# Performance work log

Hardware: AMD Instinct MI355X
Metric: run time of the kernel (lower is better)

Reference implementation:

```python
import jax, jax.numpy as jnp
import numpy as np

EPS = 1e-5

@jax.custom_vjp
def binarize(x):
    # sign with sign(0)->+1, as in typical BNN implementations
    return jnp.where(x >= 0, 1.0, -1.0).astype(x.dtype)

def _bin_fwd(x):
    return binarize(x), x

def _bin_bwd(x, g):
    # hardtanh straight-through estimator
    return (g * (jnp.abs(x) <= 1.0).astype(g.dtype),)

binarize.defvjp(_bin_fwd, _bin_bwd)

def bconv3x3(x, w, stride=1):
    bx = binarize(x)
    bw = binarize(w)
    return jax.lax.conv_general_dilated(
        bx, bw, window_strides=(stride, stride), padding=[(1, 1), (1, 1)],
        dimension_numbers=("NCHW", "OIHW", "NCHW"))

def bn(x, gamma, beta, mean, var):
    inv = gamma / jnp.sqrt(var + EPS)
    return x * inv[None, :, None, None] + (beta - mean * inv)[None, :, None, None]

def channel_shuffle(x, groups=2):
    b, c, h, w = x.shape
    x = x.reshape(b, groups, c // groups, h, w)
    x = jnp.transpose(x, (0, 2, 1, 3, 4))
    return x.reshape(b, c, h, w)

def hardtanh(x):
    return jnp.clip(x, -1.0, 1.0)

def setup_inputs() -> dict:
    key = jax.random.key(0)
    ks = jax.random.split(key, 13)
    P = 128
    inp = {
        "x": jax.random.normal(ks[0], (32, 2 * P, 56, 56), jnp.float32),
        "w1": jax.random.normal(ks[1], (P, P, 3, 3), jnp.float32) * 0.05,
        "w2": jax.random.normal(ks[2], (P, P, 3, 3), jnp.float32) * 0.05,
        "bn1_gamma": jax.random.uniform(ks[3], (P,), jnp.float32, 0.5, 1.5),
        "bn1_beta": jax.random.normal(ks[4], (P,), jnp.float32) * 0.1,
        "bn1_mean": jax.random.normal(ks[5], (P,), jnp.float32),
        "bn1_var": jax.random.uniform(ks[6], (P,), jnp.float32, 0.5, 1.5),
        "bn2_gamma": jax.random.uniform(ks[7], (P,), jnp.float32, 0.5, 1.5),
        "bn2_beta": jax.random.normal(ks[8], (P,), jnp.float32) * 0.1,
        "bn2_mean": jax.random.normal(ks[9], (P,), jnp.float32),
        "bn2_var": jax.random.uniform(ks[10], (P,), jnp.float32, 0.5, 1.5),
        "move0_bias": jax.random.normal(ks[11], (P,), jnp.float32) * 0.01,
        "move1_bias": jax.random.normal(ks[12], (P,), jnp.float32) * 0.01,
    }
    return inp

def reference(x, w1, w2, bn1_gamma, bn1_beta, bn1_mean, bn1_var,
              bn2_gamma, bn2_beta, bn2_mean, bn2_var, move0_bias, move1_bias):
    P = w1.shape[0]
    # split into active / idle halves
    x_act, x_idle = x[:, :P], x[:, P:]
    residual = x_act
    out = bn(bconv3x3(x_act, w1, stride=1), bn1_gamma, bn1_beta, bn1_mean, bn1_var)
    out = hardtanh(out + residual)
    x_idle = x_idle + move0_bias[None, :, None, None]
    out = channel_shuffle(jnp.concatenate([out, x_idle], axis=1))
    x_act2, x_idle2 = out[:, :P], out[:, P:]
    residual = x_act2
    out = bn(bconv3x3(x_act2, w2, stride=1), bn2_gamma, bn2_beta, bn2_mean, bn2_var)
    out = hardtanh(out + residual)
    x_idle2 = x_idle2 + move1_bias[None, :, None, None]
    out = channel_shuffle(jnp.concatenate([out, x_idle2], axis=1))
    return out
```

## Files before the change

kernel.cpp:

```cpp
#include <hip/hip_runtime.h>
#include <stdint.h>


#define HH 56
#define WW 56
#define HW 3136
#define NBATCH 32
#define NPX (NBATCH * HW)

#define WS_W1B   0u
#define WS_W2B   18432u
#define WS_BN    36864u
#define WS_BITS2 40960u
#define WS_BITS1 1646592u
#define WS_RES1  3252224u

#define PC(a,b) (__popc((a).x ^ (b).x) + __popc((a).y ^ (b).y) + \
                 __popc((a).z ^ (b).z) + __popc((a).w ^ (b).w))

__global__ __launch_bounds__(256) void binpack_kernel(
    const float* __restrict__ x, const float* __restrict__ move0,
    const float* __restrict__ move1,
    const float* __restrict__ w1, const float* __restrict__ w2,
    const float* __restrict__ g1, const float* __restrict__ b1,
    const float* __restrict__ m1, const float* __restrict__ v1,
    const float* __restrict__ g2, const float* __restrict__ b2,
    const float* __restrict__ m2, const float* __restrict__ v2,
    uint4* __restrict__ bits1, uint4* __restrict__ bits2,
    uint4* __restrict__ w1b, uint4* __restrict__ w2b, float* __restrict__ bnc,
    float* __restrict__ out)
{
    if (blockIdx.x >= 1960) {
        int t = (blockIdx.x - 1960) * 256 + threadIdx.x;
        if (t < 2304) {
            const float* w = (t < 1152) ? w1 : w2;
            uint4* dst = (t < 1152) ? w1b : w2b;
            int tt = (t < 1152) ? t : t - 1152;
            int o = tt / 9, tap = tt % 9;
            const float* wp = w + (size_t)o * 1152 + tap;
            uint32_t b[4];
            #pragma unroll
            for (int wd = 0; wd < 4; ++wd) {
                uint32_t acc = 0;
                #pragma unroll
                for (int bi = 0; bi < 32; ++bi) {
                    float wv = wp[(size_t)(wd * 32 + bi) * 9];
                    acc |= (wv >= 0.0f ? 1u : 0u) << bi;
                }
                b[wd] = acc;
            }
            dst[o * 9 + tap] = make_uint4(b[0], b[1], b[2], b[3]);
        } else if (t < 2432) {
            int c = t - 2304;
            float i1 = __fdiv_rn(g1[c], __fsqrt_rn(__fadd_rn(v1[c], 1e-5f)));
            bnc[c]       = i1;
            bnc[128 + c] = __fsub_rn(b1[c], __fmul_rn(m1[c], i1));
            float i2 = __fdiv_rn(g2[c], __fsqrt_rn(__fadd_rn(v2[c], 1e-5f)));
            bnc[256 + c] = i2;
            bnc[384 + c] = __fsub_rn(b2[c], __fmul_rn(m2[c], i2));
        }
        return;
    }

    const int g = blockIdx.x / 392;
    const int px = (blockIdx.x % 392) * 256 + threadIdx.x;
    const int n = px / HW, poff = px % HW;
    const float* xn = x + (size_t)n * 256 * HW + poff;

    if (g < 2) {
        const int cb = g * 64;
        uint32_t w0 = 0, w1v = 0;
        #pragma unroll
        for (int c = 0; c < 32; ++c)
            w0 |= (xn[(size_t)(cb + c) * HW] >= 0.0f ? 1u : 0u) << c;
        #pragma unroll
        for (int c = 0; c < 32; ++c)
            w1v |= (xn[(size_t)(cb + 32 + c) * HW] >= 0.0f ? 1u : 0u) << c;
        ((uint2*)&bits1[px])[g] = make_uint2(w0, w1v);
    } else if (g == 2) {
        uint32_t w0 = 0, w1v = 0, w2v = 0, w3 = 0;
        #pragma unroll
        for (int k = 0; k < 64; ++k) {
            float s = __fadd_rn(xn[(size_t)(128 + k) * HW], move0[k]);
            uint32_t m = (s >= 0.0f ? 1u : 0u) << (2 * (k & 15) + 1);
            if ((k >> 4) == 0) w0 |= m; else if ((k >> 4) == 1) w1v |= m;
            else if ((k >> 4) == 2) w2v |= m; else w3 |= m;
        }
        bits2[px] = make_uint4(w0, w1v, w2v, w3);
    } else {
        const int mb = (g - 3) * 32;
        for (int mm = 0; mm < 32; ++mm) {
            int m = mb + mm;
            float v = __fadd_rn(__fadd_rn(xn[(size_t)(192 + m) * HW],
                                          move0[64 + m]), move1[2 * m + 1]);
            __builtin_nontemporal_store(v,
                &out[(size_t)(n * 256 + 4 * m + 3) * HW + poff]);
        }
    }
}


__device__ __forceinline__ int clampi(int v, int lo, int hi) {
    return v < lo ? lo : (v > hi ? hi : v);
}

__global__ __launch_bounds__(256) void conv1_kernel(
    const float* __restrict__ x, const uint4* __restrict__ w1b,
    const float* __restrict__ bnc, const float* __restrict__ move1,
    const uint4* __restrict__ bits1, uint4* __restrict__ bits2,
    uint2* __restrict__ res1, float* __restrict__ out)
{
    const int b = blockIdx.x;
    const int js = b & 15;
    const int px = (b >> 4) * 256 + threadIdx.x;
    const int n = px / HW, poff = px % HW;

    const float* xn = x + (size_t)n * 256 * HW;
    const size_t pxi = (size_t)px;
    const uint4* __restrict__ wjs = w1b + js * 72;

    float rres[8];
    #pragma unroll
    for (int jj = 0; jj < 8; ++jj)
        rres[jj] = xn[(size_t)(js * 8 + jj) * HW + poff];
    uint32_t old16 = 0;
    if (js < 8) old16 = ((const uint16_t*)(bits2 + pxi))[js];

    const int row = poff / WW, col = poff % WW;
    const int rok0 = (row >= 1), rok2 = (row <= HH - 2);
    const int cok0 = (col >= 1), cok2 = (col <= WW - 2);
    const uint32_t rs0 = rok0 ? ~0u : 0u, rs2 = rok2 ? ~0u : 0u;
    const uint32_t csL = cok0 ? ~0u : 0u, csR = cok2 ? ~0u : 0u;
    const int nvbase = ((1 + rok0 + rok2) * (1 + cok0 + cok2)) << 7;

    const uint4* bsrc = bits1 + (size_t)n * HW;
    const uint4 i00 = bsrc[clampi(poff - 57, 0, HW - 1)];
    const uint4 i01 = bsrc[clampi(poff - 56, 0, HW - 1)];
    const uint4 i02 = bsrc[clampi(poff - 55, 0, HW - 1)];
    const uint4 i10 = bsrc[clampi(poff - 1, 0, HW - 1)];
    const uint4 i11 = bsrc[poff];
    const uint4 i12 = bsrc[clampi(poff + 1, 0, HW - 1)];
    const uint4 i20 = bsrc[clampi(poff + 55, 0, HW - 1)];
    const uint4 i21 = bsrc[clampi(poff + 56, 0, HW - 1)];
    const uint4 i22 = bsrc[clampi(poff + 57, 0, HW - 1)];

    uint32_t bw = old16;
    uint32_t q0 = 0, q1 = 0;

    #pragma unroll
    for (int jj = 0; jj < 8; ++jj) {
        const int j = js * 8 + jj;
        int acc = 0;
        acc += PC(wjs[jj * 9 + 0], i00) & (int)(rs0 & csL);
        acc += PC(wjs[jj * 9 + 1], i01) & (int)rs0;
        acc += PC(wjs[jj * 9 + 2], i02) & (int)(rs0 & csR);
        acc += PC(wjs[jj * 9 + 3], i10) & (int)csL;
        acc += PC(wjs[jj * 9 + 4], i11);
        acc += PC(wjs[jj * 9 + 5], i12) & (int)csR;
        acc += PC(wjs[jj * 9 + 6], i20) & (int)(rs2 & csL);
        acc += PC(wjs[jj * 9 + 7], i21) & (int)rs2;
        acc += PC(wjs[jj * 9 + 8], i22) & (int)(rs2 & csR);
        float convf = (float)(nvbase - (acc << 1));
        float bno = __fadd_rn(__fmul_rn(convf, bnc[j]), bnc[128 + j]);
        float v2 = __fadd_rn(bno, rres[jj]);
        float vc = fminf(fmaxf(v2, -1.0f), 1.0f);
        if (js < 8) {
            bw |= (v2 >= 0.0f ? 1u : 0u) << (2 * jj);
            uint32_t q = (uint32_t)(uint8_t)(int8_t)__float2int_rn(
                __fmul_rn(vc, 127.0f));
            uint32_t sh = 8 * (jj & 3);
            if (jj < 4) q0 |= q << sh; else q1 |= q << sh;
        } else {
            int m = j - 64;
            __builtin_nontemporal_store(__fadd_rn(vc, move1[2 * m]),
                &out[(size_t)(n * 256 + 4 * m + 1) * HW + poff]);
        }
    }
    if (js < 8) {
        res1[(size_t)js * NPX + pxi] = make_uint2(q0, q1);
        ((uint16_t*)(bits2 + pxi))[js] = (uint16_t)bw;
    }
}

__global__ __launch_bounds__(256) void conv2_kernel(
    const float* __restrict__ x, const uint4* __restrict__ w2b,
    const float* __restrict__ bnc, const float* __restrict__ move0,
    const uint4* __restrict__ bits2, const uint2* __restrict__ res1,
    float* __restrict__ out)
{
    const int b = blockIdx.x;
    const int js = b & 15;
    const int px = (b >> 4) * 256 + threadIdx.x;
    const int n = px / HW, poff = px % HW;

    const float* xn = x + (size_t)n * 256 * HW;
    const size_t pxi = (size_t)px;
    const uint4* __restrict__ wjs = w2b + js * 72;

    const uint32_t rq = ((const uint32_t*)(res1 + (size_t)(js >> 1) * NPX + pxi))[js & 1];
    float ro[4];
    #pragma unroll
    for (int k = 0; k < 4; ++k)
        ro[k] = xn[(size_t)(128 + js * 4 + k) * HW + poff];

    const int row = poff / WW, col = poff % WW;
    const int rok0 = (row >= 1), rok2 = (row <= HH - 2);
    const int cok0 = (col >= 1), cok2 = (col <= WW - 2);
    const uint32_t rs0 = rok0 ? ~0u : 0u, rs2 = rok2 ? ~0u : 0u;
    const uint32_t csL = cok0 ? ~0u : 0u, csR = cok2 ? ~0u : 0u;
    const int nvbase = ((1 + rok0 + rok2) * (1 + cok0 + cok2)) << 7;

    const uint4* bsrc = bits2 + (size_t)n * HW;
    const uint4 i00 = bsrc[clampi(poff - 57, 0, HW - 1)];
    const uint4 i01 = bsrc[clampi(poff - 56, 0, HW - 1)];
    const uint4 i02 = bsrc[clampi(poff - 55, 0, HW - 1)];
    const uint4 i10 = bsrc[clampi(poff - 1, 0, HW - 1)];
    const uint4 i11 = bsrc[poff];
    const uint4 i12 = bsrc[clampi(poff + 1, 0, HW - 1)];
    const uint4 i20 = bsrc[clampi(poff + 55, 0, HW - 1)];
    const uint4 i21 = bsrc[clampi(poff + 56, 0, HW - 1)];
    const uint4 i22 = bsrc[clampi(poff + 57, 0, HW - 1)];

    #pragma unroll
    for (int jj = 0; jj < 8; ++jj) {
        const int j = js * 8 + jj;
        int acc = 0;
        acc += PC(wjs[jj * 9 + 0], i00) & (int)(rs0 & csL);
        acc += PC(wjs[jj * 9 + 1], i01) & (int)rs0;
        acc += PC(wjs[jj * 9 + 2], i02) & (int)(rs0 & csR);
        acc += PC(wjs[jj * 9 + 3], i10) & (int)csL;
        acc += PC(wjs[jj * 9 + 4], i11);
        acc += PC(wjs[jj * 9 + 5], i12) & (int)csR;
        acc += PC(wjs[jj * 9 + 6], i20) & (int)(rs2 & csL);
        acc += PC(wjs[jj * 9 + 7], i21) & (int)rs2;
        acc += PC(wjs[jj * 9 + 8], i22) & (int)(rs2 & csR);
        float convf = (float)(nvbase - (acc << 1));
        float bno = __fadd_rn(__fmul_rn(convf, bnc[256 + j]), bnc[384 + j]);
        float resv;
        if (jj & 1) {
            resv = __fadd_rn(ro[jj >> 1], move0[j >> 1]);
        } else {
            int8_t q = (int8_t)(uint8_t)(rq >> (8 * (jj >> 1)));
            resv = __fmul_rn(__int2float_rn((int)q), 1.0f / 127.0f);
        }
        float v2 = __fadd_rn(bno, resv);
        float vc = fminf(fmaxf(v2, -1.0f), 1.0f);
        __builtin_nontemporal_store(vc,
            &out[(size_t)(n * 256 + 2 * j) * HW + poff]);
    }
}

extern "C" void kernel_launch(void* const* d_in, const int* in_sizes, int n_in,
                              void* d_out, int out_size, void* d_ws, size_t ws_size,
                              hipStream_t stream)
{
    const float* x   = (const float*)d_in[0];
    const float* w1  = (const float*)d_in[1];
    const float* w2  = (const float*)d_in[2];
    const float* g1  = (const float*)d_in[3];
    const float* b1  = (const float*)d_in[4];
    const float* m1  = (const float*)d_in[5];
    const float* v1  = (const float*)d_in[6];
    const float* g2  = (const float*)d_in[7];
    const float* b2  = (const float*)d_in[8];
    const float* m2  = (const float*)d_in[9];
    const float* v2  = (const float*)d_in[10];
    const float* mv0 = (const float*)d_in[11];
    const float* mv1 = (const float*)d_in[12];

    uint8_t* ws = (uint8_t*)d_ws;
    uint4* w1b = (uint4*)(ws + WS_W1B);
    uint4* w2b = (uint4*)(ws + WS_W2B);
    float* bnc = (float*)(ws + WS_BN);
    uint4* bits2 = (uint4*)(ws + WS_BITS2);
    uint4* bits1 = (uint4*)(ws + WS_BITS1);
    uint2* res1 = (uint2*)(ws + WS_RES1);
    float* outp = (float*)d_out;

    hipLaunchKernelGGL(binpack_kernel, dim3(392 * 5 + 10), dim3(256), 0, stream,
                       x, mv0, mv1, w1, w2, g1, b1, m1, v1, g2, b2, m2, v2,
                       bits1, bits2, w1b, w2b, bnc, outp);
    hipLaunchKernelGGL(conv1_kernel, dim3(392 * 16), dim3(256), 0, stream,
                       x, w1b, bnc, mv1, bits1, bits2, res1, outp);
    hipLaunchKernelGGL(conv2_kernel, dim3(392 * 16), dim3(256), 0, stream,
                       x, w2b, bnc, mv0, bits2, res1, outp);
}
```

Baseline: 105.3 us.

## Move idle-half binarization and passthrough copy from binpack into conv kernels

The binpack kernel now only packs the first 128 channels into bits1. The idle-half sign bits that feed bits2 are computed inside conv1, which reads x channels 128-191 directly, so it no longer has to read and merge a partially written bits2. The passthrough channels 192-255 are written by conv2. This removes a read-modify-write of bits2 and makes binpack a smaller launch. The cost is extra global loads in the conv kernels, which are already doing many loads.

New measurement: 98.92 us (median of 3 runs). 6.1% less time.

```diff
diff --git a/kernel.cpp b/kernel.cpp
--- a/kernel.cpp
+++ b/kernel.cpp
@@ -19,19 +19,17 @@
                  __popc((a).z ^ (b).z) + __popc((a).w ^ (b).w))
 
 __global__ __launch_bounds__(256) void binpack_kernel(
-    const float* __restrict__ x, const float* __restrict__ move0,
-    const float* __restrict__ move1,
+    const float* __restrict__ x,
     const float* __restrict__ w1, const float* __restrict__ w2,
     const float* __restrict__ g1, const float* __restrict__ b1,
     const float* __restrict__ m1, const float* __restrict__ v1,
     const float* __restrict__ g2, const float* __restrict__ b2,
     const float* __restrict__ m2, const float* __restrict__ v2,
-    uint4* __restrict__ bits1, uint4* __restrict__ bits2,
-    uint4* __restrict__ w1b, uint4* __restrict__ w2b, float* __restrict__ bnc,
-    float* __restrict__ out)
-{
-    if (blockIdx.x >= 1960) {
-        int t = (blockIdx.x - 1960) * 256 + threadIdx.x;
+    uint4* __restrict__ bits1,
+    uint4* __restrict__ w1b, uint4* __restrict__ w2b, float* __restrict__ bnc)
+{
+    if (blockIdx.x >= 784) {
+        int t = (blockIdx.x - 784) * 256 + threadIdx.x;
         if (t < 2304) {
             const float* w = (t < 1152) ? w1 : w2;
             uint4* dst = (t < 1152) ? w1b : w2b;
@@ -67,36 +65,15 @@
     const int n = px / HW, poff = px % HW;
     const float* xn = x + (size_t)n * 256 * HW + poff;
 
-    if (g < 2) {
-        const int cb = g * 64;
-        uint32_t w0 = 0, w1v = 0;
-        #pragma unroll
-        for (int c = 0; c < 32; ++c)
-            w0 |= (xn[(size_t)(cb + c) * HW] >= 0.0f ? 1u : 0u) << c;
-        #pragma unroll
-        for (int c = 0; c < 32; ++c)
-            w1v |= (xn[(size_t)(cb + 32 + c) * HW] >= 0.0f ? 1u : 0u) << c;
-        ((uint2*)&bits1[px])[g] = make_uint2(w0, w1v);
-    } else if (g == 2) {
-        uint32_t w0 = 0, w1v = 0, w2v = 0, w3 = 0;
-        #pragma unroll
-        for (int k = 0; k < 64; ++k) {
-            float s = __fadd_rn(xn[(size_t)(128 + k) * HW], move0[k]);
-            uint32_t m = (s >= 0.0f ? 1u : 0u) << (2 * (k & 15) + 1);
-            if ((k >> 4) == 0) w0 |= m; else if ((k >> 4) == 1) w1v |= m;
-            else if ((k >> 4) == 2) w2v |= m; else w3 |= m;
-        }
-        bits2[px] = make_uint4(w0, w1v, w2v, w3);
-    } else {
-        const int mb = (g - 3) * 32;
-        for (int mm = 0; mm < 32; ++mm) {
-            int m = mb + mm;
-            float v = __fadd_rn(__fadd_rn(xn[(size_t)(192 + m) * HW],
-                                          move0[64 + m]), move1[2 * m + 1]);
-            __builtin_nontemporal_store(v,
-                &out[(size_t)(n * 256 + 4 * m + 3) * HW + poff]);
-        }
-    }
+    const int cb = g * 64;
+    uint32_t w0 = 0, w1v = 0;
+    #pragma unroll
+    for (int c = 0; c < 32; ++c)
+        w0 |= (xn[(size_t)(cb + c) * HW] >= 0.0f ? 1u : 0u) << c;
+    #pragma unroll
+    for (int c = 0; c < 32; ++c)
+        w1v |= (xn[(size_t)(cb + 32 + c) * HW] >= 0.0f ? 1u : 0u) << c;
+    ((uint2*)&bits1[px])[g] = make_uint2(w0, w1v);
 }
 
 
@@ -106,7 +83,8 @@
 
 __global__ __launch_bounds__(256) void conv1_kernel(
     const float* __restrict__ x, const uint4* __restrict__ w1b,
-    const float* __restrict__ bnc, const float* __restrict__ move1,
+    const float* __restrict__ bnc, const float* __restrict__ move0,
+    const float* __restrict__ move1,
     const uint4* __restrict__ bits1, uint4* __restrict__ bits2,
     uint2* __restrict__ res1, float* __restrict__ out)
 {
@@ -123,8 +101,12 @@
     #pragma unroll
     for (int jj = 0; jj < 8; ++jj)
         rres[jj] = xn[(size_t)(js * 8 + jj) * HW + poff];
-    uint32_t old16 = 0;
-    if (js < 8) old16 = ((const uint16_t*)(bits2 + pxi))[js];
+    float xo[8];
+    if (js < 8) {
+        #pragma unroll
+        for (int jj = 0; jj < 8; ++jj)
+            xo[jj] = xn[(size_t)(128 + js * 8 + jj) * HW + poff];
+    }
 
     const int row = poff / WW, col = poff % WW;
     const int rok0 = (row >= 1), rok2 = (row <= HH - 2);
@@ -144,7 +126,7 @@
     const uint4 i21 = bsrc[clampi(poff + 56, 0, HW - 1)];
     const uint4 i22 = bsrc[clampi(poff + 57, 0, HW - 1)];
 
-    uint32_t bw = old16;
+    uint32_t bw = 0;
     uint32_t q0 = 0, q1 = 0;
 
     #pragma unroll
@@ -166,6 +148,8 @@
         float vc = fminf(fmaxf(v2, -1.0f), 1.0f);
         if (js < 8) {
             bw |= (v2 >= 0.0f ? 1u : 0u) << (2 * jj);
+            float s = __fadd_rn(xo[jj], move0[js * 8 + jj]);
+            bw |= (s >= 0.0f ? 1u : 0u) << (2 * jj + 1);
             uint32_t q = (uint32_t)(uint8_t)(int8_t)__float2int_rn(
                 __fmul_rn(vc, 127.0f));
             uint32_t sh = 8 * (jj & 3);
@@ -185,6 +169,7 @@
 __global__ __launch_bounds__(256) void conv2_kernel(
     const float* __restrict__ x, const uint4* __restrict__ w2b,
     const float* __restrict__ bnc, const float* __restrict__ move0,
+    const float* __restrict__ move1,
     const uint4* __restrict__ bits2, const uint2* __restrict__ res1,
     float* __restrict__ out)
 {
@@ -202,6 +187,10 @@
     #pragma unroll
     for (int k = 0; k < 4; ++k)
         ro[k] = xn[(size_t)(128 + js * 4 + k) * HW + poff];
+    float pt[4];
+    #pragma unroll
+    for (int k = 0; k < 4; ++k)
+        pt[k] = xn[(size_t)(192 + js * 4 + k) * HW + poff];
 
     const int row = poff / WW, col = poff % WW;
     const int rok0 = (row >= 1), rok2 = (row <= HH - 2);
@@ -248,6 +237,14 @@
         __builtin_nontemporal_store(vc,
             &out[(size_t)(n * 256 + 2 * j) * HW + poff]);
     }
+
+    #pragma unroll
+    for (int mm = 0; mm < 4; ++mm) {
+        int m = js * 4 + mm;
+        float v = __fadd_rn(__fadd_rn(pt[mm], move0[64 + m]), move1[2 * m + 1]);
+        __builtin_nontemporal_store(v,
+            &out[(size_t)(n * 256 + 4 * m + 3) * HW + poff]);
+    }
 }
 
 extern "C" void kernel_launch(void* const* d_in, const int* in_sizes, int n_in,
@@ -277,11 +274,11 @@
     uint2* res1 = (uint2*)(ws + WS_RES1);
     float* outp = (float*)d_out;
 
-    hipLaunchKernelGGL(binpack_kernel, dim3(392 * 5 + 10), dim3(256), 0, stream,
-                       x, mv0, mv1, w1, w2, g1, b1, m1, v1, g2, b2, m2, v2,
-                       bits1, bits2, w1b, w2b, bnc, outp);
+    hipLaunchKernelGGL(binpack_kernel, dim3(784 + 10), dim3(256), 0, stream,
+                       x, w1, w2, g1, b1, m1, v1, g2, b2, m2, v2,
+                       bits1, w1b, w2b, bnc);
     hipLaunchKernelGGL(conv1_kernel, dim3(392 * 16), dim3(256), 0, stream,
-                       x, w1b, bnc, mv1, bits1, bits2, res1, outp);
+                       x, w1b, bnc, mv0, mv1, bits1, bits2, res1, outp);
     hipLaunchKernelGGL(conv2_kernel, dim3(392 * 16), dim3(256), 0, stream,
-                       x, w2b, bnc, mv0, bits2, res1, outp);
-}
+                       x, w2b, bnc, mv0, mv1, bits2, res1, outp);
+}
```
